# Optimization experiments

Measured on AMD Instinct MI355X. Metric: run time of the kernel, lower is better.

Reference implementation:

```python
import jax, jax.numpy as jnp
import numpy as np

N = 50000        # nodes
E = 800000       # edges
F_IN = 128       # num_feature
NHID = 256
G = 64           # graphs in batch
NUM_GENE = 250
BN_EPS = 1e-5


def setup_inputs() -> dict:
    key = jax.random.key(0)
    ks = jax.random.split(key, 16)
    def w(i, shape, scale=0.05):
        return jax.random.normal(ks[i], shape, dtype=jnp.float32) * scale
    inp = {
        "x": jax.random.normal(ks[0], (N, F_IN), dtype=jnp.float32),
        "edge_index": jax.random.randint(ks[1], (2, E), 0, N, dtype=jnp.int32),
        "batch": jnp.sort(jax.random.randint(ks[2], (N,), 0, G, dtype=jnp.int32)),
        # conv1 MLP (input dim F_IN)
        "w1a": w(3, (F_IN, NHID)), "b1a": jnp.zeros((NHID,), jnp.float32),
        "w1b": w(4, (NHID, NHID)), "b1b": jnp.zeros((NHID,), jnp.float32),
        # convs 2-4 MLPs, stacked [3, ...]
        "W_in": w(5, (3, NHID, NHID)), "b_in": jnp.zeros((3, NHID), jnp.float32),
        "W_out": w(6, (3, NHID, NHID)), "b_out": jnp.zeros((3, NHID), jnp.float32),
        # BatchNorm affine params for bn1..bn4
        "gamma": jnp.ones((4, NHID), jnp.float32),
        "beta": jnp.zeros((4, NHID), jnp.float32),
        # readout head
        "lin1_w": w(7, (2 * NHID, NHID)), "lin1_b": jnp.zeros((NHID,), jnp.float32),
        "lin2_w": w(8, (NHID, NHID // 2)), "lin2_b": jnp.zeros((NHID // 2,), jnp.float32),
        "lin3_w": w(9, (NHID // 2, NUM_GENE)), "lin3_b": jnp.zeros((NUM_GENE,), jnp.float32),
    }
    return inp


def _bn(h, g, b):
    # PyG BatchNorm in training mode: batch statistics over nodes
    mu = h.mean(axis=0)
    var = jnp.mean((h - mu) ** 2, axis=0)
    return g * (h - mu) * jax.lax.rsqrt(var + BN_EPS) + b


def _gin(h, src, dst, W1, c1, W2, c2, g, b):
    # GINConv, eps=0: MLP(x_i + sum_{j->i} x_j), then BN + ReLU
    agg = jax.ops.segment_sum(h[src], dst, num_segments=N)  # [N, d] scatter-sum
    z = h + agg
    z = jnp.maximum(z @ W1 + c1, 0.0) @ W2 + c2
    return jnp.maximum(_bn(z, g, b), 0.0)


def _pool(h, batch):
    # cat([global_max_pool, global_mean_pool]) -> [G, 2*d]
    cnt = jax.ops.segment_sum(jnp.ones((N, 1), h.dtype), batch, num_segments=G)
    gap = jax.ops.segment_sum(h, batch, num_segments=G) / jnp.maximum(cnt, 1.0)
    gmp = jax.ops.segment_max(h, batch, num_segments=G)
    return jnp.concatenate([gmp, gap], axis=1)


def reference(x, edge_index, batch, w1a, b1a, w1b, b1b, W_in, b_in, W_out, b_out,
              gamma, beta, lin1_w, lin1_b, lin2_w, lin2_b, lin3_w, lin3_b):
    src, dst = edge_index[0], edge_index[1]
    h = _gin(x, src, dst, w1a, b1a, w1b, b1b, gamma[0], beta[0])
    acc = _pool(h, batch)
    for i in range(3):  # convs 2-4 (fixed small layer loop)
        h = _gin(h, src, dst, W_in[i], b_in[i], W_out[i], b_out[i], gamma[i + 1], beta[i + 1])
        acc = acc + _pool(h, batch)
    z = jnp.maximum(acc @ lin1_w + lin1_b, 0.0)
    # dropout p=0.5 is identity at inference
    z = jnp.maximum(z @ lin2_w + lin2_b, 0.0)
    y = z @ lin3_w + lin3_b  # [G, NUM_GENE]; torch.squeeze(dim=1) is a no-op here
    return y
```

## Files before the change

kernel.cpp:

```cpp
#include <hip/hip_runtime.h>
#include <hip/hip_bf16.h>

#define GNUM 64
#define BN_EPS 1e-5f

typedef unsigned short u16;
typedef unsigned int u32;
typedef __attribute__((ext_vector_type(8))) short short8;
typedef __attribute__((ext_vector_type(4))) float f32x4;

__device__ inline float bflo(u32 u) { union { u32 i; float f; } v; v.i = u << 16; return v.f; }
__device__ inline float bfhi(u32 u) { union { u32 i; float f; } v; v.i = u & 0xFFFF0000u; return v.f; }
__device__ inline u16 f2bf(float f) {
    union { float f; u32 i; } v; v.f = f;
    u32 x = v.i;
    return (u16)((x + 0x7FFFu + ((x >> 16) & 1u)) >> 16);
}
__device__ inline u32 pack2(float a, float b) { return (u32)f2bf(a) | ((u32)f2bf(b) << 16); }
__device__ inline void acc8(float* a, uint4 v) {
    a[0] += bflo(v.x); a[1] += bfhi(v.x); a[2] += bflo(v.y); a[3] += bfhi(v.y);
    a[4] += bflo(v.z); a[5] += bfhi(v.z); a[6] += bflo(v.w); a[7] += bfhi(v.w);
}

__global__ void zero_f(float* __restrict__ p, int n) {
    int i = blockIdx.x * 256 + threadIdx.x;
    if (i < n) p[i] = 0.f;
}
__global__ void zero_i(int* __restrict__ p, int n) {
    int i = blockIdx.x * 256 + threadIdx.x;
    if (i < n) p[i] = 0;
}

__global__ void deg_kernel(const int* __restrict__ dst, int* __restrict__ deg, int E) {
    int e = blockIdx.x * 256 + threadIdx.x;
    if (e < E) atomicAdd(&deg[dst[e]], 1);
}

__global__ void scan_block(const int* __restrict__ deg, int* __restrict__ part,
                           int* __restrict__ bsum, int n) {
    __shared__ int tmp[256];
    int i = blockIdx.x * 256 + threadIdx.x;
    int v = (i < n) ? deg[i] : 0;
    tmp[threadIdx.x] = v;
    __syncthreads();
    for (int off = 1; off < 256; off <<= 1) {
        int x = 0;
        if (threadIdx.x >= off) x = tmp[threadIdx.x - off];
        __syncthreads();
        tmp[threadIdx.x] += x;
        __syncthreads();
    }
    if (i < n) part[i] = tmp[threadIdx.x];
    if (threadIdx.x == 255) bsum[blockIdx.x] = tmp[255];
}

__global__ void scan_bsum(int* __restrict__ bsum, int nb) {
    __shared__ int tmp[256];
    int v = (threadIdx.x < nb) ? bsum[threadIdx.x] : 0;
    tmp[threadIdx.x] = v;
    __syncthreads();
    for (int off = 1; off < 256; off <<= 1) {
        int x = 0;
        if (threadIdx.x >= off) x = tmp[threadIdx.x - off];
        __syncthreads();
        tmp[threadIdx.x] += x;
        __syncthreads();
    }
    if (threadIdx.x < nb) bsum[threadIdx.x] = tmp[threadIdx.x];
}

__global__ void scan_fix(const int* __restrict__ part, const int* __restrict__ bsum,
                         int* __restrict__ offs, int* __restrict__ cursor, int n) {
    int i = blockIdx.x * 256 + threadIdx.x;
    if (i >= n) return;
    int add = (blockIdx.x > 0) ? bsum[blockIdx.x - 1] : 0;
    int incl = part[i] + add;
    offs[i + 1] = incl;
    cursor[i + 1] = incl;
    if (i == 0) { offs[0] = 0; cursor[0] = 0; }
}

__global__ void fill_kernel(const int* __restrict__ src, const int* __restrict__ dst,
                            int* __restrict__ cursor, int* __restrict__ eidx, int E) {
    int e = blockIdx.x * 256 + threadIdx.x;
    if (e >= E) return;
    int d = dst[e];
    int p = atomicAdd(&cursor[d], 1);
    eidx[p] = src[e];
}

__global__ void cnt_kernel(const int* __restrict__ batch, float* __restrict__ cnt, int Nn) {
    int tid = blockIdx.x * blockDim.x + threadIdx.x;
    int s = tid * 64;
    if (s >= Nn) return;
    int e = min(s + 64, Nn);
    int cur = batch[s]; int run = 0;
    for (int r = s; r < e; ++r) {
        int b = batch[r];
        if (b != cur) { atomicAdd(&cnt[cur], (float)run); cur = b; run = 0; }
        run++;
    }
    atomicAdd(&cnt[cur], (float)run);
}

__global__ void cvt_x(const float* __restrict__ x, u16* __restrict__ xb, int total4) {
    int i = blockIdx.x * 256 + threadIdx.x;
    if (i >= total4) return;
    float4 v = *(const float4*)&x[i * 4];
    uint2 o;
    o.x = pack2(v.x, v.y);
    o.y = pack2(v.z, v.w);
    *(uint2*)&xb[i * 4] = o;
}

template<int K>
__global__ void transw_frag(const float* __restrict__ W, u16* __restrict__ Wp) {
    int o = blockIdx.x * 256 + threadIdx.x;
    if (o >= K * 32) return;
    int l = o & 63;
    int q1 = o >> 6;
    int jf = q1 & 7;
    int q2 = q1 >> 3;
    const int KC = K / 32;
    int kc = q2 & (KC - 1);
    int t = q2 / KC;
    int kbase = kc * 32 + ((l >> 4) << 3);
    int col = t * 128 + jf * 16 + (l & 15);
#pragma unroll
    for (int e = 0; e < 8; ++e)
        Wp[(size_t)o * 8 + e] = f2bf(W[(size_t)(kbase + e) * 256 + col]);
}

template<int F>
__global__ __launch_bounds__(256)
void agg3(const u16* __restrict__ h, const int* __restrict__ offs,
          const int* __restrict__ eidx, u16* __restrict__ z, int Nn) {
    const int CH = F / 8;
    const int G = 64 / CH;
    int lane = threadIdx.x & 63;
    int n = blockIdx.x * 4 + (threadIdx.x >> 6);
    if (n >= Nn) return;
    int cc = lane & (CH - 1);
    int g = lane / CH;
    const u16* hp = h + cc * 8;

    float a[8] = {0.f, 0.f, 0.f, 0.f, 0.f, 0.f, 0.f, 0.f};
    if (g == 0) acc8(a, *(const uint4*)&hp[(size_t)n * F]);

    int j1 = offs[n + 1];
    int j = offs[n] + g;
    for (; j + 3 * G < j1; j += 4 * G) {
        int s0 = eidx[j], s1 = eidx[j + G], s2 = eidx[j + 2 * G], s3 = eidx[j + 3 * G];
        uint4 v0 = *(const uint4*)&hp[(size_t)s0 * F];
        uint4 v1 = *(const uint4*)&hp[(size_t)s1 * F];
        uint4 v2 = *(const uint4*)&hp[(size_t)s2 * F];
        uint4 v3 = *(const uint4*)&hp[(size_t)s3 * F];
        acc8(a, v0); acc8(a, v1); acc8(a, v2); acc8(a, v3);
    }
    for (; j < j1; j += G) {
        uint4 v = *(const uint4*)&hp[(size_t)eidx[j] * F];
        acc8(a, v);
    }
#pragma unroll
    for (int off = 32; off >= CH; off >>= 1)
#pragma unroll
        for (int e = 0; e < 8; ++e) a[e] += __shfl_down(a[e], off, 64);
    if (g == 0) {
        uint4 o;
        o.x = pack2(a[0], a[1]); o.y = pack2(a[2], a[3]);
        o.z = pack2(a[4], a[5]); o.w = pack2(a[6], a[7]);
        *(uint4*)&z[(size_t)n * F + cc * 8] = o;
    }
}

template<int K, bool RELU, bool STATS>
__global__ __launch_bounds__(256, 4)
void gemm_mfma(const u16* __restrict__ A, const u16* __restrict__ Wp,
               const float* __restrict__ bias, u16* __restrict__ C,
               float* __restrict__ stats, int M) {
    constexpr int KC = K / 32;
    __shared__ u16 As[64 * K];
    __shared__ u16 tbuf[4608];
    __shared__ float cs[256];
    int t = threadIdx.x;
    int lane = t & 63, wave = t >> 6;
    int m0 = blockIdx.x * 64;
    int n0 = blockIdx.y * 128;
    int wm = (wave & 1) << 5;
    int wn = (wave >> 1) << 6;
    int lm = lane & 15, q = lane >> 4;

    {
        int row = t >> 2, s = t & 3;
        int gr = m0 + row; if (gr >= M) gr = M - 1;
        const u16* gp = A + (size_t)gr * K + s * (K / 4);
        int mf = row >> 4, r15 = row & 15;
#pragma unroll
        for (int j = 0; j < K / 32; ++j) {
            uint4 v = *(const uint4*)(gp + j * 8);
            int c = s * (K / 32) + j;
            int kc = c >> 2, qq = c & 3;
            *(uint4*)&As[((mf * KC + kc) * 64 + r15 + (qq << 4)) * 8] = v;
        }
    }
    __syncthreads();

    f32x4 acc[2][4];
#pragma unroll
    for (int i = 0; i < 2; ++i)
#pragma unroll
        for (int j = 0; j < 4; ++j) acc[i][j] = (f32x4)0.0f;

    const u16* bbase = Wp + ((size_t)blockIdx.y * KC * 512
                             + (((wave >> 1) << 2) * 64) + lane) * 8;
    int mfb = (wave & 1) << 1;

    short8 a0[2], a1[2], b0[4], b1[4];
#pragma unroll
    for (int i = 0; i < 2; ++i)
        a0[i] = *(const short8*)&As[((mfb + i) * KC + 0) * 512 + lane * 8];
#pragma unroll
    for (int j = 0; j < 4; ++j) b0[j] = *(const short8*)(bbase + j * 512);

#pragma unroll
    for (int kc = 0; kc < KC; ++kc) {
        short8* ac = (kc & 1) ? a1 : a0;
        short8* bc = (kc & 1) ? b1 : b0;
        short8* an = (kc & 1) ? a0 : a1;
        short8* bn = (kc & 1) ? b0 : b1;
        if (kc + 1 < KC) {
#pragma unroll
            for (int i = 0; i < 2; ++i)
                an[i] = *(const short8*)&As[((mfb + i) * KC + kc + 1) * 512 + lane * 8];
#pragma unroll
            for (int j = 0; j < 4; ++j)
                bn[j] = *(const short8*)(bbase + (size_t)(kc + 1) * 4096 + j * 512);
        }
#pragma unroll
        for (int i = 0; i < 2; ++i)
#pragma unroll
            for (int j = 0; j < 4; ++j)
                acc[i][j] = __builtin_amdgcn_mfma_f32_16x16x32_bf16(ac[i], bc[j], acc[i][j], 0, 0, 0);
    }

    float bv[4], s_sum[4], s_sq[4];
#pragma unroll
    for (int j = 0; j < 4; ++j) {
        bv[j] = bias[n0 + wn + j * 16 + lm];
        s_sum[j] = 0.f; s_sq[j] = 0.f;
    }
#pragma unroll
    for (int i = 0; i < 2; ++i) {
#pragma unroll
        for (int j = 0; j < 4; ++j) {
#pragma unroll
            for (int r = 0; r < 4; ++r) {
                int row = m0 + wm + i * 16 + q * 4 + r;
                float v = acc[i][j][r] + bv[j];
                if (RELU) v = fmaxf(v, 0.f);
                if (STATS && row < M) { s_sum[j] += v; s_sq[j] = fmaf(v, v, s_sq[j]); }
                tbuf[wave * 1152 + (q * 4 + r) * 72 + j * 16 + lm] = f2bf(v);
            }
        }
        __syncthreads();
        int rl = lane >> 2, seg = lane & 3;
        uint4 w0 = *(const uint4*)&tbuf[wave * 1152 + rl * 72 + seg * 16];
        uint4 w1 = *(const uint4*)&tbuf[wave * 1152 + rl * 72 + seg * 16 + 8];
        int rowg = m0 + wm + i * 16 + rl;
        if (rowg < M) {
            u16* cp = C + (size_t)rowg * 256 + n0 + wn + seg * 16;
            *(uint4*)cp = w0;
            *(uint4*)(cp + 8) = w1;
        }
        __syncthreads();
    }

    if (STATS) {
        cs[t] = 0.f;
        __syncthreads();
#pragma unroll
        for (int j = 0; j < 4; ++j) {
            int lc = wn + j * 16 + lm;
            atomicAdd(&cs[lc], s_sum[j]);
            atomicAdd(&cs[128 + lc], s_sq[j]);
        }
        __syncthreads();
        if (t < 128)      atomicAdd(&stats[n0 + t], cs[t]);
        else              atomicAdd(&stats[256 + n0 + (t - 128)], cs[t]);
    }
}

__global__ __launch_bounds__(256)
void bn_pool(const u16* __restrict__ Z, const float* __restrict__ stats,
             const float* __restrict__ gamma, const float* __restrict__ beta,
             const int* __restrict__ batch, u16* __restrict__ H,
             float* __restrict__ pool_max, float* __restrict__ pool_sum, int Nn) {
    int col = threadIdx.x;
    int r0 = blockIdx.x * 64;
    if (r0 >= Nn) return;
    float mu = stats[col] / (float)Nn;
    float var = stats[256 + col] / (float)Nn - mu * mu;
    float scale = gamma[col] * rsqrtf(var + BN_EPS);
    float shift = beta[col] - mu * scale;
    int rend = min(r0 + 64, Nn);
    int cur = batch[r0];
    float rmax = 0.f, rsum = 0.f;
    for (int r = r0; r < rend; ++r) {
        int bb = batch[r];
        if (bb != cur) {
            atomicMax((int*)&pool_max[cur * 256 + col], __float_as_int(rmax));
            atomicAdd(&pool_sum[cur * 256 + col], rsum);
            cur = bb; rmax = 0.f; rsum = 0.f;
        }
        float v = fmaf(bflo(Z[(size_t)r * 256 + col]), scale, shift);
        v = fmaxf(v, 0.f);
        H[(size_t)r * 256 + col] = f2bf(v);
        rmax = fmaxf(rmax, v); rsum += v;
    }
    atomicMax((int*)&pool_max[cur * 256 + col], __float_as_int(rmax));
    atomicAdd(&pool_sum[cur * 256 + col], rsum);
}

__global__ void acc_update(float* __restrict__ pmax, float* __restrict__ psum,
                           const float* __restrict__ cnt, float* __restrict__ acc,
                           float* __restrict__ stats) {
    int i = blockIdx.x * 256 + threadIdx.x;
    int g = i >> 9, c = i & 511;
    float v;
    if (c < 256) {
        v = pmax[g * 256 + c];
        pmax[g * 256 + c] = 0.f;
    } else {
        int cc = c - 256;
        v = psum[g * 256 + cc] / fmaxf(cnt[g], 1.f);
        psum[g * 256 + cc] = 0.f;
    }
    acc[i] += v;
    if (i < 512) stats[i] = 0.f;
}

__global__ __launch_bounds__(256)
void readout_kernel(const float* __restrict__ acc,
                    const float* __restrict__ w1, const float* __restrict__ b1,
                    const float* __restrict__ w2, const float* __restrict__ b2,
                    const float* __restrict__ w3, const float* __restrict__ b3,
                    float* __restrict__ out) {
    __shared__ float a[512], z1[256], z2[128];
    int g = blockIdx.x, t = threadIdx.x;
    a[t] = acc[g * 512 + t];
    a[t + 256] = acc[g * 512 + 256 + t];
    __syncthreads();
    float s = b1[t];
    for (int k = 0; k < 512; ++k) s = fmaf(a[k], w1[k * 256 + t], s);
    z1[t] = fmaxf(s, 0.f);
    __syncthreads();
    if (t < 128) {
        float s2 = b2[t];
        for (int k = 0; k < 256; ++k) s2 = fmaf(z1[k], w2[k * 128 + t], s2);
        z2[t] = fmaxf(s2, 0.f);
    }
    __syncthreads();
    if (t < 250) {
        float s3 = b3[t];
        for (int k = 0; k < 128; ++k) s3 = fmaf(z2[k], w3[k * 250 + t], s3);
        out[g * 250 + t] = s3;
    }
}

extern "C" void kernel_launch(void* const* d_in, const int* in_sizes, int n_in,
                              void* d_out, int out_size, void* d_ws, size_t ws_size,
                              hipStream_t stream) {
    const float* x     = (const float*)d_in[0];
    const int* ei      = (const int*)d_in[1];
    const int* batch   = (const int*)d_in[2];
    const float* w1a   = (const float*)d_in[3];
    const float* b1a   = (const float*)d_in[4];
    const float* w1b   = (const float*)d_in[5];
    const float* b1b   = (const float*)d_in[6];
    const float* W_in  = (const float*)d_in[7];
    const float* b_in  = (const float*)d_in[8];
    const float* W_out = (const float*)d_in[9];
    const float* b_out = (const float*)d_in[10];
    const float* gamma = (const float*)d_in[11];
    const float* beta  = (const float*)d_in[12];
    const float* l1w   = (const float*)d_in[13];
    const float* l1b   = (const float*)d_in[14];
    const float* l2w   = (const float*)d_in[15];
    const float* l2b   = (const float*)d_in[16];
    const float* l3w   = (const float*)d_in[17];
    const float* l3b   = (const float*)d_in[18];

    const int N = in_sizes[2];
    const int E = in_sizes[1] / 2;
    const int* srcv = ei;
    const int* dstv = ei + E;

    u16* B0 = (u16*)d_ws;
    u16* B1 = B0 + (size_t)N * 256;
    u16* B2 = B1 + (size_t)N * 256;
    u16* Xb = B1;
    u16* Wp = B2 + (size_t)N * 256;
    float* stats = (float*)(Wp + 32768 + 7 * 65536);
    float* pmax  = stats + 512;
    float* psum  = pmax + GNUM * 256;
    float* acc   = psum + GNUM * 256;
    float* cnt   = acc + GNUM * 512;
    int* deg    = (int*)(cnt + GNUM);
    int* part   = deg + N;
    int* bsum   = part + N;
    int* offs   = bsum + 256;
    int* cursor = offs + N + 1;
    int* eidx   = cursor + N + 1;

    int nb256 = (N + 255) / 256;
    int nbM   = (N + 63) / 64;
    int nb64  = (N + 63) / 64;
    int nbW   = (N + 3) / 4;
    int eb    = (E + 255) / 256;
    const int FTOT = 512 + GNUM * 256 * 2 + GNUM * 512 + GNUM;

    zero_i<<<nb256, 256, 0, stream>>>(deg, N);
    zero_f<<<(FTOT + 255) / 256, 256, 0, stream>>>(stats, FTOT);
    deg_kernel<<<eb, 256, 0, stream>>>(dstv, deg, E);
    scan_block<<<nb256, 256, 0, stream>>>(deg, part, bsum, N);
    scan_bsum<<<1, 256, 0, stream>>>(bsum, nb256);
    scan_fix<<<nb256, 256, 0, stream>>>(part, bsum, offs, cursor, N);
    fill_kernel<<<eb, 256, 0, stream>>>(srcv, dstv, cursor, eidx, E);
    cnt_kernel<<<(nb64 + 255) / 256, 256, 0, stream>>>(batch, cnt, N);

    cvt_x<<<(N * 128 / 4 + 255) / 256, 256, 0, stream>>>(x, Xb, N * 128 / 4);
    u16* Wp1 = Wp + 32768;
    transw_frag<128><<<(128 * 32 + 255) / 256, 256, 0, stream>>>(w1a, Wp);
    transw_frag<256><<<(256 * 32 + 255) / 256, 256, 0, stream>>>(w1b, Wp1);
    for (int i = 0; i < 3; ++i) {
        transw_frag<256><<<(256 * 32 + 255) / 256, 256, 0, stream>>>(
            W_in + (size_t)i * 65536, Wp1 + (size_t)(1 + i) * 65536);
        transw_frag<256><<<(256 * 32 + 255) / 256, 256, 0, stream>>>(
            W_out + (size_t)i * 65536, Wp1 + (size_t)(4 + i) * 65536);
    }

    for (int L = 0; L < 4; ++L) {
        if (L == 0) {
            agg3<128><<<nbW, 256, 0, stream>>>(Xb, offs, eidx, B0, N);
            gemm_mfma<128, true, false><<<dim3(nbM, 2), 256, 0, stream>>>(
                B0, Wp, b1a, B1, nullptr, N);
            gemm_mfma<256, false, true><<<dim3(nbM, 2), 256, 0, stream>>>(
                B1, Wp1, b1b, B0, stats, N);
        } else {
            agg3<256><<<nbW, 256, 0, stream>>>(B2, offs, eidx, B0, N);
            gemm_mfma<256, true, false><<<dim3(nbM, 2), 256, 0, stream>>>(
                B0, Wp1 + (size_t)(1 + L - 1) * 65536, b_in + (L - 1) * 256, B1, nullptr, N);
            gemm_mfma<256, false, true><<<dim3(nbM, 2), 256, 0, stream>>>(
                B1, Wp1 + (size_t)(4 + L - 1) * 65536, b_out + (L - 1) * 256, B0, stats, N);
        }
        bn_pool<<<nb64, 256, 0, stream>>>(B0, stats, gamma + L * 256, beta + L * 256,
                                          batch, B2, pmax, psum, N);
        acc_update<<<(GNUM * 512) / 256, 256, 0, stream>>>(pmax, psum, cnt, acc, stats);
    }
    readout_kernel<<<GNUM, 256, 0, stream>>>(acc, l1w, l1b, l2w, l2b, l3w, l3b,
                                             (float*)d_out);
}
```

Before: 858.5 us.

## Fuse the two GIN MLP GEMMs into one kernel with the hidden tile in LDS

Replaces the two separate MFMA GEMM launches per layer with a single kernel. Each block computes a 64-row tile across all 256 output columns, stores the ReLU'd hidden activations in shared memory, and runs the second GEMM from there. This removes the global write and re-read of the intermediate hidden matrix and one launch per layer. The cost is much more LDS per block (lower occupancy, launch bounds 2), a full-width weight read per block, and in-place output for layers 2-4 (reads B0 and writes B0).

```diff
diff --git a/kernel.cpp b/kernel.cpp
--- a/kernel.cpp
+++ b/kernel.cpp
@@ -173,92 +173,139 @@
     }
 }
 
-template<int K, bool RELU, bool STATS>
-__global__ __launch_bounds__(256, 4)
-void gemm_mfma(const u16* __restrict__ A, const u16* __restrict__ Wp,
-               const float* __restrict__ bias, u16* __restrict__ C,
-               float* __restrict__ stats, int M) {
-    constexpr int KC = K / 32;
-    __shared__ u16 As[64 * K];
+template<int K1>
+__global__ __launch_bounds__(256, 2)
+void gin_mlp(const u16* __restrict__ Z, const u16* __restrict__ W1p,
+             const float* __restrict__ b1, const u16* __restrict__ W2p,
+             const float* __restrict__ b2, u16* __restrict__ Cout,
+             float* __restrict__ stats, int M) {
+    constexpr int KC1 = K1 / 32;
+    __shared__ u16 As[64 * K1];
+    __shared__ u16 Hs[64 * 256];
     __shared__ u16 tbuf[4608];
     __shared__ float cs[256];
     int t = threadIdx.x;
     int lane = t & 63, wave = t >> 6;
     int m0 = blockIdx.x * 64;
-    int n0 = blockIdx.y * 128;
-    int wm = (wave & 1) << 5;
-    int wn = (wave >> 1) << 6;
     int lm = lane & 15, q = lane >> 4;
 
     {
         int row = t >> 2, s = t & 3;
         int gr = m0 + row; if (gr >= M) gr = M - 1;
-        const u16* gp = A + (size_t)gr * K + s * (K / 4);
+        const u16* gp = Z + (size_t)gr * K1 + s * (K1 / 4);
         int mf = row >> 4, r15 = row & 15;
 #pragma unroll
-        for (int j = 0; j < K / 32; ++j) {
+        for (int j = 0; j < K1 / 32; ++j) {
             uint4 v = *(const uint4*)(gp + j * 8);
-            int c = s * (K / 32) + j;
+            int c = s * (K1 / 32) + j;
             int kc = c >> 2, qq = c & 3;
-            *(uint4*)&As[((mf * KC + kc) * 64 + r15 + (qq << 4)) * 8] = v;
-        }
-    }
-    __syncthreads();
-
-    f32x4 acc[2][4];
-#pragma unroll
-    for (int i = 0; i < 2; ++i)
+            *(uint4*)&As[((mf * KC1 + kc) * 64 + r15 + (qq << 4)) * 8] = v;
+        }
+    }
+    __syncthreads();
+
+    f32x4 acc[4][4];
+#pragma unroll
+    for (int i = 0; i < 4; ++i)
 #pragma unroll
         for (int j = 0; j < 4; ++j) acc[i][j] = (f32x4)0.0f;
 
-    const u16* bbase = Wp + ((size_t)blockIdx.y * KC * 512
-                             + (((wave >> 1) << 2) * 64) + lane) * 8;
-    int mfb = (wave & 1) << 1;
-
-    short8 a0[2], a1[2], b0[4], b1[4];
-#pragma unroll
-    for (int i = 0; i < 2; ++i)
-        a0[i] = *(const short8*)&As[((mfb + i) * KC + 0) * 512 + lane * 8];
-#pragma unroll
-    for (int j = 0; j < 4; ++j) b0[j] = *(const short8*)(bbase + j * 512);
-
-#pragma unroll
-    for (int kc = 0; kc < KC; ++kc) {
-        short8* ac = (kc & 1) ? a1 : a0;
-        short8* bc = (kc & 1) ? b1 : b0;
-        short8* an = (kc & 1) ? a0 : a1;
-        short8* bn = (kc & 1) ? b0 : b1;
-        if (kc + 1 < KC) {
-#pragma unroll
-            for (int i = 0; i < 2; ++i)
-                an[i] = *(const short8*)&As[((mfb + i) * KC + kc + 1) * 512 + lane * 8];
-#pragma unroll
-            for (int j = 0; j < 4; ++j)
-                bn[j] = *(const short8*)(bbase + (size_t)(kc + 1) * 4096 + j * 512);
-        }
-#pragma unroll
-        for (int i = 0; i < 2; ++i)
-#pragma unroll
-            for (int j = 0; j < 4; ++j)
-                acc[i][j] = __builtin_amdgcn_mfma_f32_16x16x32_bf16(ac[i], bc[j], acc[i][j], 0, 0, 0);
-    }
-
-    float bv[4], s_sum[4], s_sq[4];
+    {
+        const u16* bbase = W1p + ((((size_t)(wave >> 1) * KC1) * 8 + ((wave & 1) << 2)) * 64 + lane) * 8;
+        short8 a0[4], a1[4], b0[4], b1r[4];
+#pragma unroll
+        for (int i = 0; i < 4; ++i) a0[i] = *(const short8*)&As[(i * KC1) * 512 + lane * 8];
+#pragma unroll
+        for (int j = 0; j < 4; ++j) b0[j] = *(const short8*)(bbase + j * 512);
+#pragma unroll
+        for (int kc = 0; kc < KC1; ++kc) {
+            short8* ac = (kc & 1) ? a1 : a0;
+            short8* bc = (kc & 1) ? b1r : b0;
+            short8* an = (kc & 1) ? a0 : a1;
+            short8* bn = (kc & 1) ? b0 : b1r;
+            if (kc + 1 < KC1) {
+#pragma unroll
+                for (int i = 0; i < 4; ++i)
+                    an[i] = *(const short8*)&As[(i * KC1 + kc + 1) * 512 + lane * 8];
+#pragma unroll
+                for (int j = 0; j < 4; ++j)
+                    bn[j] = *(const short8*)(bbase + (size_t)(kc + 1) * 4096 + j * 512);
+            }
+#pragma unroll
+            for (int i = 0; i < 4; ++i)
+#pragma unroll
+                for (int j = 0; j < 4; ++j)
+                    acc[i][j] = __builtin_amdgcn_mfma_f32_16x16x32_bf16(ac[i], bc[j], acc[i][j], 0, 0, 0);
+        }
+    }
+
+    {
+#pragma unroll
+        for (int j = 0; j < 4; ++j) {
+            float bv = b1[wave * 64 + j * 16 + lm];
+            int kc = wave * 2 + (j >> 1);
+            int qq = ((j & 1) << 1) + (lm >> 3);
+            int e = lm & 7;
+#pragma unroll
+            for (int i = 0; i < 4; ++i) {
+#pragma unroll
+                for (int r = 0; r < 4; ++r) {
+                    float v = fmaxf(acc[i][j][r] + bv, 0.f);
+                    Hs[(((i * 8 + kc) * 64) + (q * 4 + r) + qq * 16) * 8 + e] = f2bf(v);
+                }
+            }
+        }
+    }
+    __syncthreads();
+
+#pragma unroll
+    for (int i = 0; i < 4; ++i)
+#pragma unroll
+        for (int j = 0; j < 4; ++j) acc[i][j] = (f32x4)0.0f;
+    {
+        const u16* bbase = W2p + ((((size_t)(wave >> 1) * 8) * 8 + ((wave & 1) << 2)) * 64 + lane) * 8;
+        short8 a0[4], a1[4], b0[4], b1r[4];
+#pragma unroll
+        for (int i = 0; i < 4; ++i) a0[i] = *(const short8*)&Hs[(i * 8) * 512 + lane * 8];
+#pragma unroll
+        for (int j = 0; j < 4; ++j) b0[j] = *(const short8*)(bbase + j * 512);
+#pragma unroll
+        for (int kc = 0; kc < 8; ++kc) {
+            short8* ac = (kc & 1) ? a1 : a0;
+            short8* bc = (kc & 1) ? b1r : b0;
+            short8* an = (kc & 1) ? a0 : a1;
+            short8* bn = (kc & 1) ? b0 : b1r;
+            if (kc + 1 < 8) {
+#pragma unroll
+                for (int i = 0; i < 4; ++i)
+                    an[i] = *(const short8*)&Hs[(i * 8 + kc + 1) * 512 + lane * 8];
+#pragma unroll
+                for (int j = 0; j < 4; ++j)
+                    bn[j] = *(const short8*)(bbase + (size_t)(kc + 1) * 4096 + j * 512);
+            }
+#pragma unroll
+            for (int i = 0; i < 4; ++i)
+#pragma unroll
+                for (int j = 0; j < 4; ++j)
+                    acc[i][j] = __builtin_amdgcn_mfma_f32_16x16x32_bf16(ac[i], bc[j], acc[i][j], 0, 0, 0);
+        }
+    }
+
+    float bv2[4], s_sum[4], s_sq[4];
 #pragma unroll
     for (int j = 0; j < 4; ++j) {
-        bv[j] = bias[n0 + wn + j * 16 + lm];
+        bv2[j] = b2[wave * 64 + j * 16 + lm];
         s_sum[j] = 0.f; s_sq[j] = 0.f;
     }
 #pragma unroll
-    for (int i = 0; i < 2; ++i) {
+    for (int i = 0; i < 4; ++i) {
 #pragma unroll
         for (int j = 0; j < 4; ++j) {
 #pragma unroll
             for (int r = 0; r < 4; ++r) {
-                int row = m0 + wm + i * 16 + q * 4 + r;
-                float v = acc[i][j][r] + bv[j];
-                if (RELU) v = fmaxf(v, 0.f);
-                if (STATS && row < M) { s_sum[j] += v; s_sq[j] = fmaf(v, v, s_sq[j]); }
+                int row = m0 + i * 16 + q * 4 + r;
+                float v = acc[i][j][r] + bv2[j];
+                if (row < M) { s_sum[j] += v; s_sq[j] = fmaf(v, v, s_sq[j]); }
                 tbuf[wave * 1152 + (q * 4 + r) * 72 + j * 16 + lm] = f2bf(v);
             }
         }
@@ -266,28 +313,34 @@
         int rl = lane >> 2, seg = lane & 3;
         uint4 w0 = *(const uint4*)&tbuf[wave * 1152 + rl * 72 + seg * 16];
         uint4 w1 = *(const uint4*)&tbuf[wave * 1152 + rl * 72 + seg * 16 + 8];
-        int rowg = m0 + wm + i * 16 + rl;
+        int rowg = m0 + i * 16 + rl;
         if (rowg < M) {
-            u16* cp = C + (size_t)rowg * 256 + n0 + wn + seg * 16;
+            u16* cp = Cout + (size_t)rowg * 256 + wave * 64 + seg * 16;
             *(uint4*)cp = w0;
             *(uint4*)(cp + 8) = w1;
         }
         __syncthreads();
     }
 
-    if (STATS) {
-        cs[t] = 0.f;
-        __syncthreads();
-#pragma unroll
-        for (int j = 0; j < 4; ++j) {
-            int lc = wn + j * 16 + lm;
-            atomicAdd(&cs[lc], s_sum[j]);
-            atomicAdd(&cs[128 + lc], s_sq[j]);
-        }
-        __syncthreads();
-        if (t < 128)      atomicAdd(&stats[n0 + t], cs[t]);
-        else              atomicAdd(&stats[256 + n0 + (t - 128)], cs[t]);
-    }
+    cs[t] = 0.f;
+    __syncthreads();
+#pragma unroll
+    for (int j = 0; j < 4; ++j) {
+        int lc = wave * 64 + j * 16 + lm;
+        atomicAdd(&cs[lc], s_sum[j]);
+    }
+    __syncthreads();
+    if (t < 256) atomicAdd(&stats[t], cs[t]);
+    __syncthreads();
+    cs[t] = 0.f;
+    __syncthreads();
+#pragma unroll
+    for (int j = 0; j < 4; ++j) {
+        int lc = wave * 64 + j * 16 + lm;
+        atomicAdd(&cs[lc], s_sq[j]);
+    }
+    __syncthreads();
+    if (t < 256) atomicAdd(&stats[256 + t], cs[t]);
 }
 
 __global__ __launch_bounds__(256)
@@ -442,19 +495,17 @@
     for (int L = 0; L < 4; ++L) {
         if (L == 0) {
             agg3<128><<<nbW, 256, 0, stream>>>(Xb, offs, eidx, B0, N);
-            gemm_mfma<128, true, false><<<dim3(nbM, 2), 256, 0, stream>>>(
-                B0, Wp, b1a, B1, nullptr, N);
-            gemm_mfma<256, false, true><<<dim3(nbM, 2), 256, 0, stream>>>(
-                B1, Wp1, b1b, B0, stats, N);
+            gin_mlp<128><<<nbM, 256, 0, stream>>>(B0, Wp, b1a, Wp1, b1b, B1, stats, N);
+            bn_pool<<<nb64, 256, 0, stream>>>(B1, stats, gamma, beta,
+                                              batch, B2, pmax, psum, N);
         } else {
             agg3<256><<<nbW, 256, 0, stream>>>(B2, offs, eidx, B0, N);
-            gemm_mfma<256, true, false><<<dim3(nbM, 2), 256, 0, stream>>>(
-                B0, Wp1 + (size_t)(1 + L - 1) * 65536, b_in + (L - 1) * 256, B1, nullptr, N);
-            gemm_mfma<256, false, true><<<dim3(nbM, 2), 256, 0, stream>>>(
-                B1, Wp1 + (size_t)(4 + L - 1) * 65536, b_out + (L - 1) * 256, B0, stats, N);
-        }
-        bn_pool<<<nb64, 256, 0, stream>>>(B0, stats, gamma + L * 256, beta + L * 256,
-                                          batch, B2, pmax, psum, N);
+            gin_mlp<256><<<nbM, 256, 0, stream>>>(
+                B0, Wp1 + (size_t)(1 + L - 1) * 65536, b_in + (L - 1) * 256,
+                Wp1 + (size_t)(4 + L - 1) * 65536, b_out + (L - 1) * 256, B0, stats, N);
+            bn_pool<<<nb64, 256, 0, stream>>>(B0, stats, gamma + L * 256, beta + L * 256,
+                                              batch, B2, pmax, psum, N);
+        }
         acc_update<<<(GNUM * 512) / 256, 256, 0, stream>>>(pmax, psum, cnt, acc, stats);
     }
     readout_kernel<<<GNUM, 256, 0, stream>>>(acc, l1w, l1b, l2w, l2b, l3w, l3b,
```

Result: faster. 728.4 us (-15.2%).
